# Optimization experiments

Measured on AMD Instinct MI355X. Metric: run time of the kernel, lower is better.

## Reference

```python
import jax, jax.numpy as jnp
import numpy as np

TAU = 2.0       # LIF membrane time constant (spikingjelly default)
ALPHA = 2.0     # ATan surrogate sharpness
EPS = 1e-5      # BN eps
NUM_HEADS = 12
PATCH = 2
LENTH = 256     # (H/PATCH)*(W/PATCH)

@jax.custom_vjp
def heaviside(x):
    return (x >= 0.0).astype(x.dtype)

def _hv_fwd(x):
    return heaviside(x), x

def _hv_bwd(x, g):
    sg = ALPHA / 2.0 / (1.0 + (jnp.pi / 2.0 * ALPHA * x) ** 2)  # ATan surrogate
    return (g * sg,)

heaviside.defvjp(_hv_fwd, _hv_bwd)

def lif(x):
    # multi-step LIF over leading time axis, hard reset, v_th = 1.0
    def step(v, xt):
        v = v + (xt - v) / TAU
        s = heaviside(v - 1.0)
        return v * (1.0 - s), s
    _, s = jax.lax.scan(step, jnp.zeros_like(x[0]), x)
    return s

def setup_inputs() -> dict:
    key = jax.random.key(0)
    ks = jax.random.split(key, 9)
    T, B, C, H, W = 4, 4, 384, 32, 32
    x = jax.random.normal(ks[0], (T, B, C, H, W), dtype=jnp.float32)
    Wconv = jax.random.normal(ks[1], (2 * C, C, PATCH, PATCH), dtype=jnp.float32) * (1.0 / np.sqrt(C * PATCH * PATCH))
    gamma1 = jax.random.uniform(ks[2], (2 * C,), dtype=jnp.float32, minval=0.5, maxval=1.5)
    beta1 = jax.random.normal(ks[3], (2 * C,), dtype=jnp.float32) * 0.1
    Wproj = jax.random.normal(ks[4], (C, C), dtype=jnp.float32) * (1.0 / np.sqrt(C))
    gamma2 = jax.random.uniform(ks[5], (C,), dtype=jnp.float32, minval=0.5, maxval=1.5)
    beta2 = jax.random.normal(ks[6], (C,), dtype=jnp.float32) * 0.1
    firing_rate_x = jax.random.uniform(ks[7], (1, 1, NUM_HEADS, 1, 1), dtype=jnp.float32, minval=0.05, maxval=0.5)
    firing_rate_attn = jax.random.uniform(ks[8], (1, 1, NUM_HEADS, 1, 1), dtype=jnp.float32, minval=0.05, maxval=0.5)
    return {"x": x, "Wconv": Wconv, "gamma1": gamma1, "beta1": beta1, "Wproj": Wproj,
            "gamma2": gamma2, "beta2": beta2, "firing_rate_x": firing_rate_x,
            "firing_rate_attn": firing_rate_attn}

def reference(x, Wconv, gamma1, beta1, Wproj, gamma2, beta2, firing_rate_x, firing_rate_attn):
    T, B, C, H, W = x.shape
    d = C // NUM_HEADS
    xs = lif(x)                                          # spikes [T,B,C,H,W]
    # patch conv dim -> 2*dim, stride = kernel = PATCH (eval BN: running mean 0, var 1)
    y = jax.lax.conv_general_dilated(xs.reshape(T * B, C, H, W), Wconv,
                                     (PATCH, PATCH), 'VALID',
                                     dimension_numbers=('NCHW', 'OIHW', 'NCHW'))
    bn1 = gamma1 / jnp.sqrt(1.0 + EPS)
    y = y * bn1[None, :, None, None] + beta1[None, :, None, None]
    Np = (H // PATCH) * (W // PATCH)                     # == LENTH
    y = y.reshape(T, B, NUM_HEADS, 2 * d, Np)
    y1, y2 = y[:, :, :, :d, :], y[:, :, :, d:, :]
    xr = xs.reshape(T, B, NUM_HEADS, d, H * W)
    scale1 = 1.0 / jnp.sqrt(firing_rate_x * d)
    attn = jnp.einsum('tbhdn,tbhdm->tbhnm', y1, xr) * scale1   # [T,B,h,Np,HW]
    attn = lif(attn)
    scale2 = 1.0 / jnp.sqrt(firing_rate_attn * LENTH)
    out = jnp.einsum('tbhdn,tbhnm->tbhdm', y2, attn) * scale2  # [T,B,h,d,HW]
    out = out.reshape(T, B, C, H, W)
    out = lif(out)
    out = jnp.einsum('oc,tbchw->tbohw', Wproj, out)            # 1x1 conv proj
    bn2 = gamma2 / jnp.sqrt(1.0 + EPS)
    out = out * bn2[None, None, :, None, None] + beta2[None, None, :, None, None]
    return out + x
```

## Files before the change

kernel.cpp:

```cpp
#include <hip/hip_runtime.h>
#include <hip/hip_bf16.h>
#include <math.h>


typedef __attribute__((ext_vector_type(8))) short short8;
typedef __attribute__((ext_vector_type(4))) float f32x4;

#define T_ 4
#define B_ 4
#define C_ 384
#define HW 1024
#define NH_ 12
#define Np_ 256
#define EPS_ 1e-5f
#define LDK 56

static __device__ __forceinline__ unsigned short f2bf(float f) {
    __hip_bfloat16 h = __float2bfloat16(f);
    return *reinterpret_cast<unsigned short*>(&h);
}
static __device__ __forceinline__ float bf2f(unsigned short u) {
    __hip_bfloat16 h = *reinterpret_cast<__hip_bfloat16*>(&u);
    return __bfloat162float(h);
}
static __device__ __forceinline__ void split3(float w, unsigned short& u0,
                                              unsigned short& u1, unsigned short& u2) {
    u0 = f2bf(w);  float f0 = bf2f(u0);
    float r1 = w - f0;
    u1 = f2bf(r1); float f1 = bf2f(u1);
    u2 = f2bf(r1 - f1);
}

__global__ __launch_bounds__(256) void k_wsplit(const float* __restrict__ Wc,
                                                const float* __restrict__ Wp,
                                                unsigned short* __restrict__ Wc3,
                                                unsigned short* __restrict__ Wp3) {
    const int NC = 768 * 1536;
    const int NP = 384 * 384;
    int i = blockIdx.x * 256 + threadIdx.x;
    float w; unsigned short* dst; int idx, plane;
    if (i < NC) { w = Wc[i]; dst = Wc3; idx = i; plane = NC; }
    else {
        int j = i - NC;
        if (j >= NP) return;
        w = Wp[j]; dst = Wp3; idx = j; plane = NP;
    }
    unsigned short u0, u1, u2;
    split3(w, u0, u1, u2);
    dst[idx] = u0; dst[plane + idx] = u1; dst[2 * plane + idx] = u2;
}

__global__ __launch_bounds__(256) void k_lif_im2col(const float* __restrict__ x,
                                                    unsigned short* __restrict__ Bc,
                                                    unsigned short* __restrict__ xsb) {
    int gt = blockIdx.x * 256 + threadIdx.x;
    int pw = gt & 15, ph = (gt >> 4) & 15;
    int v = gt >> 8;
    int c = v % 384, b = v / 384;
    float v00 = 0.f, v01 = 0.f, v10 = 0.f, v11 = 0.f;
    const size_t xrow = ((size_t)b * C_ + c) * HW + (size_t)(2 * ph) * 32 + 2 * pw;
#pragma unroll
    for (int t = 0; t < T_; ++t) {
        const float* px = x + (size_t)t * (B_ * C_ * HW) + xrow;
        float2 r0 = *(const float2*)px;
        float2 r1 = *(const float2*)(px + 32);
        v00 += (r0.x - v00) * 0.5f;
        v01 += (r0.y - v01) * 0.5f;
        v10 += (r1.x - v10) * 0.5f;
        v11 += (r1.y - v11) * 0.5f;
        ushort4 s;
        s.x = (v00 >= 1.f) ? 0x3F80 : 0; if (v00 >= 1.f) v00 = 0.f;
        s.y = (v01 >= 1.f) ? 0x3F80 : 0; if (v01 >= 1.f) v01 = 0.f;
        s.z = (v10 >= 1.f) ? 0x3F80 : 0; if (v10 >= 1.f) v10 = 0.f;
        s.w = (v11 >= 1.f) ? 0x3F80 : 0; if (v11 >= 1.f) v11 = 0.f;
        int tb = t * B_ + b;
        int n = tb * 256 + ph * 16 + pw;
        *(ushort4*)(Bc + (size_t)n * 1536 + 4 * c) = s;
        size_t xo = ((size_t)tb * C_ + c) * HW + (size_t)(2 * ph) * 32 + 2 * pw;
        ushort2 w0 = {s.x, s.y}, w1 = {s.z, s.w};
        *(ushort2*)(xsb + xo) = w0;
        *(ushort2*)(xsb + xo + 32) = w1;
    }
}

#define GL16(GP, LP) __builtin_amdgcn_global_load_lds(                        \
    (const __attribute__((address_space(1))) void*)(GP),                      \
    (__attribute__((address_space(3))) void*)(LP), 16, 0, 0)

static __device__ __forceinline__ void stage_conv(const unsigned short* __restrict__ Wc3,
                                                  const unsigned short* __restrict__ Bc,
                                                  short* smb, int mb, int nb, int k0,
                                                  int wid, int rloc, int cswz) {
    if (wid == 0) {
#pragma unroll
        for (int s = 0; s < 3; ++s)
#pragma unroll
            for (int u = 0; u < 2; ++u)
                GL16(Wc3 + ((size_t)(s * 768 + mb * 32 + u * 16 + rloc)) * 1536 + k0 + cswz * 8,
                     smb + s * 1024 + u * 512);
        GL16(Bc + ((size_t)(nb * 128 + rloc)) * 1536 + k0 + cswz * 8, smb + 3072);
    } else {
#pragma unroll
        for (int v = 1; v < 8; ++v)
            GL16(Bc + ((size_t)(nb * 128 + v * 16 + rloc)) * 1536 + k0 + cswz * 8,
                 smb + 3072 + v * 512);
    }
}

__global__ __launch_bounds__(128) void k_mconv(const unsigned short* __restrict__ Bc,
                                               const unsigned short* __restrict__ Wc3,
                                               const float* __restrict__ g1,
                                               const float* __restrict__ b1,
                                               const float* __restrict__ frx,
                                               const float* __restrict__ fra,
                                               unsigned short* __restrict__ y1s,
                                               unsigned short* __restrict__ y2s) {
    __shared__ short sm[2][7168];
    const int nb = blockIdx.x, mb = blockIdx.y;
    const int tid = threadIdx.x;
    const int lane = tid & 63, wid = tid >> 6;
    const int quad = lane >> 4, lr = lane & 15;
    const int rloc = lane >> 2;
    const int cswz = (lane & 3) ^ ((lane >> 3) & 3);
    const int slot = quad ^ ((lr >> 1) & 3);
    const int wn = wid;

    f32x4 acc[2][4];
#pragma unroll
    for (int im = 0; im < 2; ++im)
#pragma unroll
        for (int in = 0; in < 4; ++in)
            acc[im][in] = (f32x4){0.f, 0.f, 0.f, 0.f};

    stage_conv(Wc3, Bc, sm[0], mb, nb, 0, wid, rloc, cswz);

#pragma unroll 2
    for (int kt = 0; kt < 48; ++kt) {
        const int b = kt & 1;
        if (kt < 47) {
            stage_conv(Wc3, Bc, sm[b ^ 1], mb, nb, (kt + 1) * 32, wid, rloc, cswz);
            asm volatile("s_waitcnt vmcnt(7)" ::: "memory");
        } else {
            asm volatile("s_waitcnt vmcnt(0)" ::: "memory");
        }
        __builtin_amdgcn_s_barrier();
        __builtin_amdgcn_sched_barrier(0);

        const short* smb = sm[b];
        short8 af[3][2], bf[4];
#pragma unroll
        for (int s = 0; s < 3; ++s)
#pragma unroll
            for (int im = 0; im < 2; ++im)
                af[s][im] = *(const short8*)&smb[s * 1024 + (im * 16 + lr) * 32 + slot * 8];
#pragma unroll
        for (int in = 0; in < 4; ++in)
            bf[in] = *(const short8*)&smb[3072 + (wn * 64 + in * 16 + lr) * 32 + slot * 8];
        asm volatile("s_waitcnt lgkmcnt(0)" ::: "memory");
        __builtin_amdgcn_sched_barrier(0);
        __builtin_amdgcn_s_barrier();
        __builtin_amdgcn_sched_barrier(0);

#pragma unroll
        for (int s = 0; s < 3; ++s)
#pragma unroll
            for (int im = 0; im < 2; ++im)
#pragma unroll
                for (int in = 0; in < 4; ++in)
                    acc[im][in] = __builtin_amdgcn_mfma_f32_16x16x32_bf16(af[s][im], bf[in], acc[im][in], 0, 0, 0);
    }

    const float rs = 1.0f / sqrtf(1.0f + EPS_);
    const int h = mb >> 1, half = mb & 1;
    const float scl = (half == 0) ? (1.0f / sqrtf(frx[h] * 32.0f))
                                  : (1.0f / sqrtf(fra[h] * 256.0f));
    unsigned short* dst = (half == 0) ? y1s : y2s;
#pragma unroll
    for (int im = 0; im < 2; ++im) {
#pragma unroll
        for (int in = 0; in < 4; ++in) {
            int n_g = nb * 128 + wn * 64 + in * 16 + lr;
            int tb = n_g >> 8, pn = n_g & 255;
            size_t base = (size_t)(tb * NH_ + h) * 3 * 8192;
            ushort4 o0, o1, o2;
#pragma unroll
            for (int r = 0; r < 4; ++r) {
                int oc = mb * 32 + im * 16 + quad * 4 + r;
                float val = (acc[im][in][r] * (g1[oc] * rs) + b1[oc]) * scl;
                unsigned short u0, u1, u2;
                split3(val, u0, u1, u2);
                ((unsigned short*)&o0)[r] = u0;
                ((unsigned short*)&o1)[r] = u1;
                ((unsigned short*)&o2)[r] = u2;
            }
            int dd = im * 16 + quad * 4;
            if (half == 0) {
                *(ushort4*)&dst[base + 0 * 8192 + (size_t)pn * 32 + dd] = o0;
                *(ushort4*)&dst[base + 1 * 8192 + (size_t)pn * 32 + dd] = o1;
                *(ushort4*)&dst[base + 2 * 8192 + (size_t)pn * 32 + dd] = o2;
            } else {
#pragma unroll
                for (int r = 0; r < 4; ++r) {
                    dst[base + 0 * 8192 + (size_t)(dd + r) * 256 + pn] = ((unsigned short*)&o0)[r];
                    dst[base + 1 * 8192 + (size_t)(dd + r) * 256 + pn] = ((unsigned short*)&o1)[r];
                    dst[base + 2 * 8192 + (size_t)(dd + r) * 256 + pn] = ((unsigned short*)&o2)[r];
                }
            }
        }
    }
}

__global__ __launch_bounds__(256, 2) void k_attn_qk(const unsigned short* __restrict__ xsb,
                                                    const unsigned short* __restrict__ y1s,
                                                    unsigned short* __restrict__ abq) {
    __shared__ unsigned short xb[4][64][40];
    const int h = blockIdx.y, b = blockIdx.z;
    const int tid = threadIdx.x;
    const int lane = tid & 63, wq = tid >> 6;
    const int quad = lane >> 4, lr = lane & 15;
    const int m0 = blockIdx.x * 64;

#pragma unroll
    for (int i = 0; i < 8; ++i) {
        int e = tid + i * 256;
        int j4 = e & 15, d = (e >> 4) & 31, t = e >> 9;
        ushort4 v = *(const ushort4*)(xsb + ((size_t)((t * B_ + b) * C_) + h * 32 + d) * HW + m0 + j4 * 4);
        xb[t][j4 * 4 + 0][d] = v.x;
        xb[t][j4 * 4 + 1][d] = v.y;
        xb[t][j4 * 4 + 2][d] = v.z;
        xb[t][j4 * 4 + 3][d] = v.w;
    }
    __syncthreads();

    float vat[4][4][4];
#pragma unroll
    for (int mi = 0; mi < 4; ++mi)
#pragma unroll
        for (int itl = 0; itl < 4; ++itl)
#pragma unroll
            for (int r = 0; r < 4; ++r) vat[mi][itl][r] = 0.f;

#pragma unroll
    for (int t = 0; t < T_; ++t) {
        const int tb = t * B_ + b;
        const size_t slab = (size_t)(tb * NH_ + h) * 3 * 8192;

        short8 af[3][4];
        const unsigned short* y1p = y1s + slab + (size_t)(wq * 64 + lr) * 32 + quad * 8;
#pragma unroll
        for (int s = 0; s < 3; ++s)
#pragma unroll
            for (int itl = 0; itl < 4; ++itl)
                af[s][itl] = *(const short8*)(y1p + s * 8192 + itl * 512);

#pragma unroll
        for (int mi = 0; mi < 4; ++mi) {
            short8 bx = *(const short8*)&xb[t][mi * 16 + lr][quad * 8];
            f32x4 acc[4];
#pragma unroll
            for (int itl = 0; itl < 4; ++itl) acc[itl] = (f32x4){0.f, 0.f, 0.f, 0.f};
#pragma unroll
            for (int s = 0; s < 3; ++s)
#pragma unroll
                for (int itl = 0; itl < 4; ++itl)
                    acc[itl] = __builtin_amdgcn_mfma_f32_16x16x32_bf16(af[s][itl], bx, acc[itl], 0, 0, 0);

            unsigned int q = 0;
#pragma unroll
            for (int itl = 0; itl < 4; ++itl)
#pragma unroll
                for (int r = 0; r < 4; ++r) {
                    float v = vat[mi][itl][r];
                    v += (acc[itl][r] - v) * 0.5f;
                    bool s = (v >= 1.0f);
                    vat[mi][itl][r] = s ? 0.f : v;
                    q |= (s ? 1u : 0u) << (itl * 4 + r);
                }
            int m = m0 + mi * 16 + lr;
            abq[(((size_t)(tb * NH_ + h) * 1024 + m) * 4 + quad) * 4 + wq] = (unsigned short)q;
        }
    }
}

__global__ __launch_bounds__(256, 1) void k_attn_pv(const unsigned long long* __restrict__ abits,
                                                    const unsigned short* __restrict__ y2s,
                                                    unsigned short* __restrict__ obt) {
    const int h = blockIdx.y, b = blockIdx.z;
    const int tid = threadIdx.x;
    const int lane = tid & 63, wv = tid >> 6;
    const int quad = lane >> 4, lr = lane & 15;
    const int dt = wv >> 1, mg = wv & 1;
    const int mbase = blockIdx.x * 128 + mg * 64;
    const int obase = (quad & 2) << 1;

    float vo[4][4];
#pragma unroll
    for (int mi = 0; mi < 4; ++mi)
#pragma unroll
        for (int r = 0; r < 4; ++r) vo[mi][r] = 0.f;

#pragma unroll
    for (int t = 0; t < T_; ++t) {
        const int tb = t * B_ + b;
        const size_t slab = (size_t)(tb * NH_ + h) * 3 * 8192;

        short8 ay[3][8];
        const unsigned short* y2p = y2s + slab + (size_t)(dt * 16 + lr) * 256 + quad * 8;
#pragma unroll
        for (int s = 0; s < 3; ++s)
#pragma unroll
            for (int kt = 0; kt < 8; ++kt)
                ay[s][kt] = *(const short8*)(y2p + s * 8192 + kt * 32);

#pragma unroll
        for (int mi = 0; mi < 4; ++mi) {
            const int m = mbase + mi * 16 + lr;
            const unsigned long long* ap = abits + ((size_t)(tb * NH_ + h) * 1024 + m) * 4 + (quad & 1) * 2;
            unsigned long long Qa = ap[0];
            unsigned long long Qb = ap[1];

            short8 bs[8];
#pragma unroll
            for (int kt = 0; kt < 8; ++kt) {
                int o = kt * 8 + obase;
                unsigned int a4 = (unsigned int)(Qa >> o) & 15u;
                unsigned int b4 = (unsigned int)(Qb >> o) & 15u;
                union { short8 v; unsigned int w[4]; } u;
                u.w[0] = ((a4 & 1u) ? 0x3F80u : 0u) | ((a4 & 2u) ? 0x3F800000u : 0u);
                u.w[1] = ((a4 & 4u) ? 0x3F80u : 0u) | ((a4 & 8u) ? 0x3F800000u : 0u);
                u.w[2] = ((b4 & 1u) ? 0x3F80u : 0u) | ((b4 & 2u) ? 0x3F800000u : 0u);
                u.w[3] = ((b4 & 4u) ? 0x3F80u : 0u) | ((b4 & 8u) ? 0x3F800000u : 0u);
                bs[kt] = u.v;
            }

            f32x4 acc2 = (f32x4){0.f, 0.f, 0.f, 0.f};
#pragma unroll
            for (int s = 0; s < 3; ++s)
#pragma unroll
                for (int kt = 0; kt < 8; ++kt)
                    acc2 = __builtin_amdgcn_mfma_f32_16x16x32_bf16(ay[s][kt], bs[kt], acc2, 0, 0, 0);

            ushort4 ob;
#pragma unroll
            for (int r = 0; r < 4; ++r) {
                float v = vo[mi][r];
                v += (acc2[r] - v) * 0.5f;
                bool s = (v >= 1.0f);
                ((unsigned short*)&ob)[r] = s ? 0x3F80 : 0;
                vo[mi][r] = s ? 0.f : v;
            }
            *(ushort4*)(obt + ((size_t)tb * HW + m) * C_ + h * 32 + dt * 16 + quad * 4) = ob;
        }
    }
}

__global__ __launch_bounds__(256) void k_mproj(const unsigned short* __restrict__ obt,
                                               const unsigned short* __restrict__ Wp3,
                                               const float* __restrict__ g2,
                                               const float* __restrict__ b2,
                                               const float* __restrict__ x,
                                               float* __restrict__ out) {
    __shared__ short As[3][64][LDK];
    __shared__ short Bs[128][LDK];
    const int nb = blockIdx.x, mb = blockIdx.y;
    const int tid = threadIdx.x;
    const int lane = tid & 63, wave = tid >> 6;
    const int wm = wave >> 1, wn = wave & 1;
    const int quad = lane >> 4, lr = lane & 15;
    const int arow = tid >> 2, akoff = (tid & 3) * 8;
    f32x4 acc[2][4];
#pragma unroll
    for (int im = 0; im < 2; ++im)
#pragma unroll
        for (int in = 0; in < 4; ++in)
            acc[im][in] = (f32x4){0.f, 0.f, 0.f, 0.f};

    for (int k0 = 0; k0 < 384; k0 += 32) {
#pragma unroll
        for (int s = 0; s < 3; ++s) {
            short8 a = *(const short8*)(Wp3 + ((size_t)(s * 384 + mb * 64 + arow)) * 384 + k0 + akoff);
            *(short8*)&As[s][arow][akoff] = a;
        }
#pragma unroll
        for (int i = 0; i < 2; ++i) {
            int f = i * 256 + tid;
            int row = f >> 2, koff = (f & 3) * 8;
            short8 bv = *(const short8*)(obt + ((size_t)(nb * 128 + row)) * 384 + k0 + koff);
            *(short8*)&Bs[row][koff] = bv;
        }
        __syncthreads();
        short8 bf[4], af[3][2];
#pragma unroll
        for (int in = 0; in < 4; ++in)
            bf[in] = *(const short8*)&Bs[wn * 64 + in * 16 + lr][quad * 8];
#pragma unroll
        for (int s = 0; s < 3; ++s)
#pragma unroll
            for (int im = 0; im < 2; ++im)
                af[s][im] = *(const short8*)&As[s][wm * 32 + im * 16 + lr][quad * 8];
#pragma unroll
        for (int s = 0; s < 3; ++s)
#pragma unroll
            for (int im = 0; im < 2; ++im)
#pragma unroll
                for (int in = 0; in < 4; ++in)
                    acc[im][in] = __builtin_amdgcn_mfma_f32_16x16x32_bf16(af[s][im], bf[in], acc[im][in], 0, 0, 0);
        __syncthreads();
    }
    const float rs = 1.0f / sqrtf(1.0f + EPS_);
#pragma unroll
    for (int im = 0; im < 2; ++im) {
#pragma unroll
        for (int in = 0; in < 4; ++in) {
            int n_g = nb * 128 + wn * 64 + in * 16 + lr;
            int tb = n_g >> 10, hw = n_g & 1023;
#pragma unroll
            for (int r = 0; r < 4; ++r) {
                int o = mb * 64 + wm * 32 + im * 16 + quad * 4 + r;
                size_t idx = ((size_t)tb * C_ + o) * HW + hw;
                out[idx] = acc[im][in][r] * (g2[o] * rs) + b2[o] + x[idx];
            }
        }
    }
}

extern "C" void kernel_launch(void* const* d_in, const int* in_sizes, int n_in,
                              void* d_out, int out_size, void* d_ws, size_t ws_size,
                              hipStream_t stream) {
    const float* x      = (const float*)d_in[0];
    const float* Wconv  = (const float*)d_in[1];
    const float* gamma1 = (const float*)d_in[2];
    const float* beta1  = (const float*)d_in[3];
    const float* Wproj  = (const float*)d_in[4];
    const float* gamma2 = (const float*)d_in[5];
    const float* beta2  = (const float*)d_in[6];
    const float* frx    = (const float*)d_in[7];
    const float* fra    = (const float*)d_in[8];
    float* out = (float*)d_out;

    unsigned short* ws16 = (unsigned short*)d_ws;
    unsigned short* Bc  = ws16;
    unsigned short* obt = ws16;
    unsigned short* Wc3 = ws16 + 6291456;
    unsigned short* Wp3 = ws16 + 9830400;
    unsigned short* xsb = ws16 + 10272768;
    unsigned short* y1s = ws16 + 16564224;
    unsigned short* y2s = ws16 + 21282816;
    unsigned long long* abits = (unsigned long long*)(ws16 + 26001408);

    k_wsplit<<<5184, 256, 0, stream>>>(Wconv, Wproj, Wc3, Wp3);
    k_lif_im2col<<<1536, 256, 0, stream>>>(x, Bc, xsb);
    k_mconv<<<dim3(32, 24), 128, 0, stream>>>(Bc, Wc3, gamma1, beta1, frx, fra, y1s, y2s);
    k_attn_qk<<<dim3(16, 12, 4), 256, 0, stream>>>(xsb, y1s, (unsigned short*)abits);
    k_attn_pv<<<dim3(8, 12, 4), 256, 0, stream>>>(abits, y2s, obt);
    k_mproj<<<dim3(128, 6), 256, 0, stream>>>(obt, Wp3, gamma2, beta2, x, out);
}
```

Measured before the change: 246.9 us.

## Load conv A fragments directly to registers and give each wave private B buffers

The merged patch-conv GEMM now loads weight (A) fragments straight from global memory into registers and double-buffers them in registers. Each wave stages only its own 64-row slice of B into a per-wave LDS region, which removes both block-wide barriers per k-step. This targets barrier stalls and the LDS round trip for A. In exchange each wave issues redundant global loads of A and holds twice as many A fragments in registers, and the vmcnt-based waits leave no cross-wave synchronization.

```diff
diff --git a/kernel.cpp b/kernel.cpp
--- a/kernel.cpp
+++ b/kernel.cpp
@@ -87,24 +87,35 @@
     (const __attribute__((address_space(1))) void*)(GP),                      \
     (__attribute__((address_space(3))) void*)(LP), 16, 0, 0)
 
-static __device__ __forceinline__ void stage_conv(const unsigned short* __restrict__ Wc3,
-                                                  const unsigned short* __restrict__ Bc,
-                                                  short* smb, int mb, int nb, int k0,
-                                                  int wid, int rloc, int cswz) {
-    if (wid == 0) {
-#pragma unroll
-        for (int s = 0; s < 3; ++s)
-#pragma unroll
-            for (int u = 0; u < 2; ++u)
-                GL16(Wc3 + ((size_t)(s * 768 + mb * 32 + u * 16 + rloc)) * 1536 + k0 + cswz * 8,
-                     smb + s * 1024 + u * 512);
-        GL16(Bc + ((size_t)(nb * 128 + rloc)) * 1536 + k0 + cswz * 8, smb + 3072);
-    } else {
-#pragma unroll
-        for (int v = 1; v < 8; ++v)
-            GL16(Bc + ((size_t)(nb * 128 + v * 16 + rloc)) * 1536 + k0 + cswz * 8,
-                 smb + 3072 + v * 512);
-    }
+static __device__ __forceinline__ void ldA(short8 af[3][2],
+                                           const unsigned short* aBase, int k0) {
+#pragma unroll
+    for (int s = 0; s < 3; ++s)
+#pragma unroll
+        for (int im = 0; im < 2; ++im)
+            af[s][im] = *(const short8*)(aBase + (size_t)(s * 768 + im * 16) * 1536 + k0);
+}
+
+static __device__ __forceinline__ void stageB(const unsigned short* bSrc,
+                                              short* bbuf, int k0) {
+#pragma unroll
+    for (int v = 0; v < 4; ++v)
+        GL16(bSrc + (size_t)v * 16 * 1536 + k0, bbuf + v * 512);
+}
+
+static __device__ __forceinline__ void mfma_step(f32x4 acc[2][4], const short8 af[3][2],
+                                                 const short* bbuf, int lr, int slot) {
+    short8 bf[4];
+#pragma unroll
+    for (int in = 0; in < 4; ++in)
+        bf[in] = *(const short8*)&bbuf[(in * 16 + lr) * 32 + slot * 8];
+#pragma unroll
+    for (int s = 0; s < 3; ++s)
+#pragma unroll
+        for (int im = 0; im < 2; ++im)
+#pragma unroll
+            for (int in = 0; in < 4; ++in)
+                acc[im][in] = __builtin_amdgcn_mfma_f32_16x16x32_bf16(af[s][im], bf[in], acc[im][in], 0, 0, 0);
 }
 
 __global__ __launch_bounds__(128) void k_mconv(const unsigned short* __restrict__ Bc,
@@ -115,7 +126,7 @@
                                                const float* __restrict__ fra,
                                                unsigned short* __restrict__ y1s,
                                                unsigned short* __restrict__ y2s) {
-    __shared__ short sm[2][7168];
+    __shared__ short bs[2][2][2048];
     const int nb = blockIdx.x, mb = blockIdx.y;
     const int tid = threadIdx.x;
     const int lane = tid & 63, wid = tid >> 6;
@@ -125,6 +136,11 @@
     const int slot = quad ^ ((lr >> 1) & 3);
     const int wn = wid;
 
+    const unsigned short* aBase = Wc3 + (size_t)(mb * 32 + lr) * 1536 + quad * 8;
+    const unsigned short* bSrc  = Bc + (size_t)(nb * 128 + wn * 64 + rloc) * 1536 + cswz * 8;
+    short* bb0 = &bs[wid][0][0];
+    short* bb1 = &bs[wid][1][0];
+
     f32x4 acc[2][4];
 #pragma unroll
     for (int im = 0; im < 2; ++im)
@@ -132,42 +148,31 @@
         for (int in = 0; in < 4; ++in)
             acc[im][in] = (f32x4){0.f, 0.f, 0.f, 0.f};
 
-    stage_conv(Wc3, Bc, sm[0], mb, nb, 0, wid, rloc, cswz);
-
-#pragma unroll 2
-    for (int kt = 0; kt < 48; ++kt) {
-        const int b = kt & 1;
-        if (kt < 47) {
-            stage_conv(Wc3, Bc, sm[b ^ 1], mb, nb, (kt + 1) * 32, wid, rloc, cswz);
-            asm volatile("s_waitcnt vmcnt(7)" ::: "memory");
-        } else {
-            asm volatile("s_waitcnt vmcnt(0)" ::: "memory");
-        }
-        __builtin_amdgcn_s_barrier();
-        __builtin_amdgcn_sched_barrier(0);
-
-        const short* smb = sm[b];
-        short8 af[3][2], bf[4];
-#pragma unroll
-        for (int s = 0; s < 3; ++s)
-#pragma unroll
-            for (int im = 0; im < 2; ++im)
-                af[s][im] = *(const short8*)&smb[s * 1024 + (im * 16 + lr) * 32 + slot * 8];
-#pragma unroll
-        for (int in = 0; in < 4; ++in)
-            bf[in] = *(const short8*)&smb[3072 + (wn * 64 + in * 16 + lr) * 32 + slot * 8];
-        asm volatile("s_waitcnt lgkmcnt(0)" ::: "memory");
-        __builtin_amdgcn_sched_barrier(0);
-        __builtin_amdgcn_s_barrier();
-        __builtin_amdgcn_sched_barrier(0);
-
-#pragma unroll
-        for (int s = 0; s < 3; ++s)
-#pragma unroll
-            for (int im = 0; im < 2; ++im)
-#pragma unroll
-                for (int in = 0; in < 4; ++in)
-                    acc[im][in] = __builtin_amdgcn_mfma_f32_16x16x32_bf16(af[s][im], bf[in], acc[im][in], 0, 0, 0);
+    short8 afA[3][2], afB[3][2];
+    ldA(afA, aBase, 0);
+    stageB(bSrc, bb0, 0);
+
+    for (int kt = 0; kt < 48; kt += 2) {
+        {
+            int kn = (kt + 1) * 32;
+            ldA(afB, aBase, kn);
+            stageB(bSrc, bb1, kn);
+            asm volatile("s_waitcnt vmcnt(10)" ::: "memory");
+            __builtin_amdgcn_sched_barrier(0);
+            mfma_step(acc, afA, bb0, lr, slot);
+        }
+        {
+            int kn = (kt + 2) * 32;
+            if (kn < 1536) {
+                ldA(afA, aBase, kn);
+                stageB(bSrc, bb0, kn);
+                asm volatile("s_waitcnt vmcnt(10)" ::: "memory");
+            } else {
+                asm volatile("s_waitcnt vmcnt(0)" ::: "memory");
+            }
+            __builtin_amdgcn_sched_barrier(0);
+            mfma_step(acc, afB, bb1, lr, slot);
+        }
     }
 
     const float rs = 1.0f / sqrtf(1.0f + EPS_);
```

After: 269.8 us. 1.09x slower.
